# Performance work log

Hardware: AMD Instinct MI355X
Metric: run time of the kernel (lower is better)

Reference implementation:

```python
import jax, jax.numpy as jnp
import numpy as np

B, S, D, H = 4, 2048, 1024, 16
E = D // H  # head_size = 64


def setup_inputs() -> dict:
    key = jax.random.key(0)
    ks = jax.random.split(key, 6)
    scale = 1.0 / np.sqrt(D)
    embedded = jax.random.normal(ks[0], (B, S, D), dtype=jnp.float32)
    # Per-head Q/K/V projection weights, stacked over heads: [H, D, E]
    Wq = jax.random.normal(ks[1], (H, D, E), dtype=jnp.float32) * scale
    Wk = jax.random.normal(ks[2], (H, D, E), dtype=jnp.float32) * scale
    Wv = jax.random.normal(ks[3], (H, D, E), dtype=jnp.float32) * scale
    # Output projection (nn.Linear(model_dim, model_dim))
    Wo = jax.random.normal(ks[4], (D, D), dtype=jnp.float32) * scale
    bo = jax.random.normal(ks[5], (D,), dtype=jnp.float32) * scale
    return {"embedded": embedded, "Wq": Wq, "Wk": Wk, "Wv": Wv, "Wo": Wo, "bo": bo}


def reference(embedded, Wq, Wk, Wv, Wo, bo):
    # Batched over heads instead of the original Python loop; same math.
    q = jnp.einsum('bsd,hde->bhse', embedded, Wq)  # [B,H,S,E]
    k = jnp.einsum('bsd,hde->bhse', embedded, Wk)
    v = jnp.einsum('bsd,hde->bhse', embedded, Wv)
    scores = jnp.einsum('bhse,bhte->bhst', q, k) / jnp.sqrt(jnp.float32(E))
    causal = jnp.tril(jnp.ones((S, S), dtype=bool))  # [S,S]
    scores = jnp.where(causal, scores, jnp.float32(-jnp.inf))
    attn = jax.nn.softmax(scores, axis=-1)  # [B,H,S,S]
    out = jnp.einsum('bhst,bhte->bhse', attn, v)  # [B,H,S,E]
    # concat heads along last dim: [B,S,H*E] == [B,S,D]
    out = out.transpose(0, 2, 1, 3).reshape(B, S, D)
    # output projection (dropout is identity in eval mode)
    return out @ Wo.T + bo
```

## Files before the change

### kernel.cpp

```cpp
#include <hip/hip_runtime.h>
#include <hip/hip_bf16.h>

#define B_ 4
#define S_ 2048
#define D_ 1024
#define H_ 16
#define E_ 64
#define M_ (B_*S_)
#define NQKV_ 3072

typedef __attribute__((ext_vector_type(8))) short bf16x8;
typedef __attribute__((ext_vector_type(4))) float f32x4;
typedef __attribute__((ext_vector_type(16))) float f32x16;
typedef __attribute__((ext_vector_type(4))) unsigned short u16x4;
typedef unsigned short u16;

#define QSCALE 0.18033688011f
#define AS1 __attribute__((address_space(1)))
#define AS3 __attribute__((address_space(3)))

#define SWZ(r) ((((r) & 7) ^ ((((r) >> 3) & 3) << 1)) << 4)

static __device__ __forceinline__ u16 f2bf(float f) {
  unsigned u = __builtin_bit_cast(unsigned, f);
  unsigned r = (u + 0x7FFFu + ((u >> 16) & 1u)) >> 16;
  return (u16)r;
}

static __device__ __forceinline__ unsigned pk2(float a, float b) {
  unsigned r;
  asm("v_cvt_pk_bf16_f32 %0, %1, %2" : "=v"(r) : "v"(a), "v"(b));
  return r;
}


__global__ __launch_bounds__(256) void cvt_fused(const float* __restrict__ emb,
                                                 const float* __restrict__ Wo,
                                                 const float* __restrict__ Wq,
                                                 const float* __restrict__ Wk,
                                                 const float* __restrict__ Wv,
                                                 u16* __restrict__ X,
                                                 u16* __restrict__ WoT,
                                                 u16* __restrict__ Wt) {
  __shared__ float t[64][65];
  const int bid = blockIdx.x;
  const int tid = threadIdx.x;
  if (bid < 8192) {
    int i = bid * 256 + tid;
    f32x4 v = ((const f32x4*)emb)[i];
    u16x4 o;
    o.x = f2bf(v.x); o.y = f2bf(v.y); o.z = f2bf(v.z); o.w = f2bf(v.w);
    ((u16x4*)X)[i] = o;
  } else if (bid < 9216) {
    int i = (bid - 8192) * 256 + tid;
    f32x4 v = ((const f32x4*)Wo)[i];
    u16x4 o;
    o.x = f2bf(v.x); o.y = f2bf(v.y); o.z = f2bf(v.z); o.w = f2bf(v.w);
    ((u16x4*)WoT)[i] = o;
  } else {
    const int blk = bid - 9216;
    const int h = blk >> 4;
    const int db = (blk & 15) * 64;
    const float* srcs[3] = {Wq, Wk, Wv};
#pragma unroll
    for (int m = 0; m < 3; ++m) {
      const float* src = srcs[m] + (size_t)h * 65536 + (size_t)db * 64;
      __syncthreads();
#pragma unroll
      for (int i = 0; i < 16; ++i) {
        int idx = i * 256 + tid;
        int d = idx >> 6, e = idx & 63;
        t[e][d] = src[d * 64 + e];
      }
      __syncthreads();
      u16* dst = Wt + (size_t)(m * 1024 + h * 64) * 1024 + db;
#pragma unroll
      for (int i = 0; i < 16; ++i) {
        int idx = i * 256 + tid;
        int e = idx >> 6, d = idx & 63;
        dst[(size_t)e * 1024 + d] = f2bf(t[e][d]);
      }
    }
  }
}


__global__ __launch_bounds__(512, 2) void gemm_qkv(const u16* __restrict__ A,
                                                   const u16* __restrict__ Bt,
                                                   u16* __restrict__ QK,
                                                   u16* __restrict__ Vt) {
  __shared__ u16 As[3][256 * 32];
  __shared__ u16 Bs[3][384 * 32];
  const int tid = threadIdx.x;
  const int lane = tid & 63, wv = tid >> 6;
  const int ll = lane & 15, lg = lane >> 4;
  const int wm = wv >> 2, wn = wv & 3;
  const int bm = blockIdx.x, bn = blockIdx.y;

  const int sr = tid >> 2;
  const int scb = (tid & 3) * 16;
  const char* a0 = (const char*)(A + (size_t)(bm * 256 + sr) * 1024) + scb;
  const char* a1 = (const char*)(A + (size_t)(bm * 256 + 128 + sr) * 1024) + scb;
  const char* b0 = (const char*)(Bt + (size_t)(bn * 384 + sr) * 1024) + scb;
  const char* b1 = (const char*)(Bt + (size_t)(bn * 384 + 128 + sr) * 1024) + scb;
  const char* b2 = (const char*)(Bt + (size_t)(bn * 384 + 256 + sr) * 1024) + scb;

  auto stage = [&](int t, int bi) {
    const size_t adv = (size_t)t * 64;
    char* ad = (char*)&As[bi][0] + tid * 16;
    char* bd = (char*)&Bs[bi][0] + tid * 16;
    __builtin_amdgcn_global_load_lds((const AS1 void*)(a0 + adv), (AS3 void*)ad, 16, 0, 0);
    __builtin_amdgcn_global_load_lds((const AS1 void*)(a1 + adv), (AS3 void*)(ad + 8192), 16, 0, 0);
    __builtin_amdgcn_global_load_lds((const AS1 void*)(b0 + adv), (AS3 void*)bd, 16, 0, 0);
    __builtin_amdgcn_global_load_lds((const AS1 void*)(b1 + adv), (AS3 void*)(bd + 8192), 16, 0, 0);
    __builtin_amdgcn_global_load_lds((const AS1 void*)(b2 + adv), (AS3 void*)(bd + 16384), 16, 0, 0);
  };

  f32x4 acc[8][6] = {};

  stage(0, 0);
  stage(1, 1);
  for (int t = 0; t < 32; ++t) {
    const int cur = t % 3;
    if (t + 2 < 32) {
      stage(t + 2, (t + 2) % 3);
      asm volatile("s_waitcnt vmcnt(10)" ::: "memory");
    } else if (t + 1 < 32) {
      asm volatile("s_waitcnt vmcnt(5)" ::: "memory");
    } else {
      asm volatile("s_waitcnt vmcnt(0)" ::: "memory");
    }
    __builtin_amdgcn_s_barrier();

    const char* ab = (const char*)&As[cur][0];
    const char* bb = (const char*)&Bs[cur][0];

    bf16x8 bf[6];
#pragma unroll
    for (int ni = 0; ni < 6; ++ni) {
      int row = wn * 96 + ni * 16 + ll;
      bf[ni] = *(const bf16x8*)(bb + row * 64 + lg * 16);
    }
    __builtin_amdgcn_s_setprio(1);
#pragma unroll
    for (int mi = 0; mi < 8; ++mi) {
      int row = wm * 128 + mi * 16 + ll;
      bf16x8 af = *(const bf16x8*)(ab + row * 64 + lg * 16);
#pragma unroll
      for (int ni = 0; ni < 6; ++ni)
        acc[mi][ni] = __builtin_amdgcn_mfma_f32_16x16x32_bf16(
            af, bf[ni], acc[mi][ni], 0, 0, 0);
    }
    __builtin_amdgcn_s_setprio(0);
    __builtin_amdgcn_s_barrier();
  }

  const int sig = (((lg & 1) << 1) | (lg >> 1)) << 2;
#pragma unroll
  for (int mi = 0; mi < 8; ++mi) {
#pragma unroll
    for (int ni = 0; ni < 6; ++ni) {
      int c = bn * 384 + wn * 96 + ni * 16 + ll;
      int r0 = bm * 256 + wm * 128 + mi * 16 + lg * 4;
      if (c >= 2048) {
        int bb2 = r0 >> 11, s0 = r0 & 2047;
        int s0p = (s0 & ~15) | sig;
        u16x4 pkv;
        pkv.x = f2bf(acc[mi][ni][0]); pkv.y = f2bf(acc[mi][ni][1]);
        pkv.z = f2bf(acc[mi][ni][2]); pkv.w = f2bf(acc[mi][ni][3]);
        *(u16x4*)&Vt[((size_t)(bb2 * 1024 + (c - 2048))) * 2048 + s0p] = pkv;
      } else {
        const float qs = (c < 1024) ? QSCALE : 1.0f;
#pragma unroll
        for (int j = 0; j < 4; ++j)
          QK[(size_t)(r0 + j) * 2048 + c] = f2bf(acc[mi][ni][j] * qs);
      }
    }
  }
}


__global__ __launch_bounds__(512, 2) void gemm_out(const u16* __restrict__ A,
                                                   const u16* __restrict__ Bt,
                                                   float* __restrict__ C,
                                                   const float* __restrict__ bias) {
  __shared__ u16 As[3][256 * 32];
  __shared__ u16 Bs[3][128 * 32];
  const int tid = threadIdx.x;
  const int lane = tid & 63, wv = tid >> 6;
  const int ll = lane & 15, lg = lane >> 4;
  const int wm = wv >> 2, wn = wv & 3;
  const int bm = blockIdx.x, bn = blockIdx.y;

  const int sr = tid >> 2;
  const int scb = (tid & 3) * 16;
  const char* a0 = (const char*)(A + (size_t)(bm * 256 + sr) * 1024) + scb;
  const char* a1 = (const char*)(A + (size_t)(bm * 256 + 128 + sr) * 1024) + scb;
  const char* b0 = (const char*)(Bt + (size_t)(bn * 128 + sr) * 1024) + scb;

  auto stage = [&](int t, int bi) {
    const size_t adv = (size_t)t * 64;
    char* ad = (char*)&As[bi][0] + tid * 16;
    char* bd = (char*)&Bs[bi][0] + tid * 16;
    __builtin_amdgcn_global_load_lds((const AS1 void*)(a0 + adv), (AS3 void*)ad, 16, 0, 0);
    __builtin_amdgcn_global_load_lds((const AS1 void*)(a1 + adv), (AS3 void*)(ad + 8192), 16, 0, 0);
    __builtin_amdgcn_global_load_lds((const AS1 void*)(b0 + adv), (AS3 void*)bd, 16, 0, 0);
  };

  f32x4 acc[8][2] = {};

  stage(0, 0);
  stage(1, 1);
  for (int t = 0; t < 32; ++t) {
    const int cur = t % 3;
    if (t + 2 < 32) {
      stage(t + 2, (t + 2) % 3);
      asm volatile("s_waitcnt vmcnt(6)" ::: "memory");
    } else if (t + 1 < 32) {
      asm volatile("s_waitcnt vmcnt(3)" ::: "memory");
    } else {
      asm volatile("s_waitcnt vmcnt(0)" ::: "memory");
    }
    __builtin_amdgcn_s_barrier();

    const char* ab = (const char*)&As[cur][0];
    const char* bb = (const char*)&Bs[cur][0];

    bf16x8 bf[2];
#pragma unroll
    for (int ni = 0; ni < 2; ++ni) {
      int row = wn * 32 + ni * 16 + ll;
      bf[ni] = *(const bf16x8*)(bb + row * 64 + lg * 16);
    }
    __builtin_amdgcn_s_setprio(1);
#pragma unroll
    for (int mi = 0; mi < 8; ++mi) {
      int row = wm * 128 + mi * 16 + ll;
      bf16x8 af = *(const bf16x8*)(ab + row * 64 + lg * 16);
#pragma unroll
      for (int ni = 0; ni < 2; ++ni)
        acc[mi][ni] = __builtin_amdgcn_mfma_f32_16x16x32_bf16(
            af, bf[ni], acc[mi][ni], 0, 0, 0);
    }
    __builtin_amdgcn_s_setprio(0);
    __builtin_amdgcn_s_barrier();
  }

#pragma unroll
  for (int mi = 0; mi < 8; ++mi) {
#pragma unroll
    for (int ni = 0; ni < 2; ++ni) {
      int c = bn * 128 + wn * 32 + ni * 16 + ll;
      int r0 = bm * 256 + wm * 128 + mi * 16 + lg * 4;
      float bv = bias[c];
#pragma unroll
      for (int j = 0; j < 4; ++j)
        C[(size_t)(r0 + j) * 1024 + c] = acc[mi][ni][j] + bv;
    }
  }
}


__global__ __launch_bounds__(512, 2) void attn(const u16* __restrict__ QK,
                                               const u16* __restrict__ Vt,
                                               u16* __restrict__ AO) {
  __shared__ u16 Klds[4][4096];
  __shared__ u16 Vlds[4][4096];

  const int wg = blockIdx.x;
  const int lin = (wg & 7) * 32 + (wg >> 3);
  const int bh = lin >> 2, pr = lin & 3;
  const int b = bh >> 4, h = bh & 15;
  const int tid = threadIdx.x;
  const int lane = tid & 63, wv = tid >> 6;
  const int lq = lane & 31, hi = lane >> 5;

  const int srow = tid >> 3;
  const int scolb = ((tid & 7) * 16) ^ SWZ(srow);
  const char* ksrc = (const char*)(QK + (size_t)(b * S_ + srow) * 2048 + 1024 + h * E_) + scolb;
  const char* vsrc = (const char*)(Vt + (size_t)(bh * 64 + srow) * 2048) + scolb;

  const int nktA = 4 * pr + 4;
  const int NS = 36;

  auto stage = [&](int sq, int kb) {
    char* kd = (char*)&Klds[0][0] + (sq & 3) * 8192 + wv * 1024;
    char* vd = (char*)&Vlds[0][0] + (sq & 3) * 8192 + wv * 1024;
    __builtin_amdgcn_global_load_lds((const AS1 void*)(ksrc + (size_t)kb * 4096),
                                     (AS3 void*)kd, 16, 0, 0);
    __builtin_amdgcn_global_load_lds((const AS1 void*)(vsrc + kb * 2),
                                     (AS3 void*)vd, 16, 0, 0);
  };

  stage(0, 0);
  stage(1, (1 < nktA ? 1 : 1 - nktA) * 64);

  int seq = 0;
  for (int ph = 0; ph < 2; ++ph) {
    const int qt = ph ? 7 - pr : pr;
    const int nkt = 4 * qt + 4;
    const int qw0 = qt * 256 + wv * 32;
    const int q = qw0 + lq;

    const u16* qp = QK + (size_t)(b * S_ + q) * 2048 + h * E_;
    bf16x8 qf[4];
#pragma unroll
    for (int c = 0; c < 4; ++c)
      qf[c] = *(const bf16x8*)(qp + c * 16 + hi * 8);

    float m_run = -INFINITY, l_part = 0.f;
    f32x16 o0 = {}, o1 = {};

    for (int kt = 0; kt < nkt; ++kt, ++seq) {
      if (seq + 2 < NS) {
        int s2 = seq + 2;
        stage(s2, (s2 < nktA ? s2 : s2 - nktA) * 64);
      }
      if (seq < NS - 2)       asm volatile("s_waitcnt vmcnt(4)" ::: "memory");
      else if (seq == NS - 2) asm volatile("s_waitcnt vmcnt(2)" ::: "memory");
      else                    asm volatile("s_waitcnt vmcnt(0)" ::: "memory");
      __builtin_amdgcn_s_barrier();

      const int kb = kt * 64;
      if (kb > qw0 + 31) continue;
      const char* kbuf = (const char*)&Klds[0][0] + (seq & 3) * 8192;
      const char* vbuf = (const char*)&Vlds[0][0] + (seq & 3) * 8192;

      auto half = [&](int kb2) __attribute__((always_inline)) {
        f32x16 sc = {};
        __builtin_amdgcn_s_setprio(1);
        const int krow = kb2 * 32 + lq;
#pragma unroll
        for (int c = 0; c < 4; ++c) {
          bf16x8 kf = *(const bf16x8*)(kbuf + krow * 128 +
                                       ((c * 32 + hi * 16) ^ SWZ(krow)));
          sc = __builtin_amdgcn_mfma_f32_32x32x16_bf16(kf, qf[c], sc, 0, 0, 0);
        }
        __builtin_amdgcn_s_setprio(0);

        if (kb + kb2 * 32 + 31 > qw0) {
#pragma unroll
          for (int r = 0; r < 16; ++r) {
            int key = kb + kb2 * 32 + (r & 3) + 8 * (r >> 2) + 4 * hi;
            if (key > q) sc[r] = -1e30f;
          }
        }

        float pm = sc[0];
#pragma unroll
        for (int r = 1; r < 16; ++r) pm = fmaxf(pm, sc[r]);
        if (__any(pm - m_run > 8.0f)) {
          float g = fmaxf(pm, __shfl_xor(pm, 32, 64));
          float mn = fmaxf(m_run, g);
          float corr = exp2f(m_run - mn);
          m_run = mn;
          l_part *= corr;
          o0 *= corr;
          o1 *= corr;
        }

        float p[16];
#pragma unroll
        for (int r = 0; r < 16; ++r) {
          p[r] = exp2f(sc[r] - m_run);
          l_part += p[r];
        }
        __builtin_amdgcn_s_setprio(1);
#pragma unroll
        for (int gg = 0; gg < 2; ++gg) {
          union { unsigned w[4]; bf16x8 v; } pf;
          pf.w[0] = pk2(p[gg * 8 + 0], p[gg * 8 + 1]);
          pf.w[1] = pk2(p[gg * 8 + 2], p[gg * 8 + 3]);
          pf.w[2] = pk2(p[gg * 8 + 4], p[gg * 8 + 5]);
          pf.w[3] = pk2(p[gg * 8 + 6], p[gg * 8 + 7]);
          const int g = kb2 * 2 + gg;
          {
            bf16x8 vf = *(const bf16x8*)(vbuf + lq * 128 +
                                         ((g * 32 + hi * 16) ^ SWZ(lq)));
            o0 = __builtin_amdgcn_mfma_f32_32x32x16_bf16(vf, pf.v, o0, 0, 0, 0);
          }
          {
            const int er = 32 + lq;
            bf16x8 vf = *(const bf16x8*)(vbuf + er * 128 +
                                         ((g * 32 + hi * 16) ^ SWZ(er)));
            o1 = __builtin_amdgcn_mfma_f32_32x32x16_bf16(vf, pf.v, o1, 0, 0, 0);
          }
        }
        __builtin_amdgcn_s_setprio(0);
      };

      half(0);
      if (kb + 32 <= qw0 + 31) half(1);
    }

    float l = l_part + __shfl_xor(l_part, 32, 64);
    float rl = 1.0f / l;

#pragma unroll
    for (int qd = 0; qd < 4; ++qd) {
      u16x4 w0, w1;
#pragma unroll
      for (int j = 0; j < 4; ++j) {
        w0[j] = f2bf(o0[qd * 4 + j] * rl);
        w1[j] = f2bf(o1[qd * 4 + j] * rl);
      }
      const size_t base = (size_t)(b * S_ + q) * D_ + h * E_ + 8 * qd + 4 * hi;
      *(u16x4*)&AO[base] = w0;
      *(u16x4*)&AO[base + 32] = w1;
    }
  }
}


extern "C" void kernel_launch(void* const* d_in, const int* in_sizes, int n_in,
                              void* d_out, int out_size, void* d_ws, size_t ws_size,
                              hipStream_t stream) {
  const float* embedded = (const float*)d_in[0];
  const float* Wq = (const float*)d_in[1];
  const float* Wk = (const float*)d_in[2];
  const float* Wv = (const float*)d_in[3];
  const float* Wo = (const float*)d_in[4];
  const float* bo = (const float*)d_in[5];
  float* out = (float*)d_out;

  char* ws = (char*)d_ws;
  u16* X    = (u16*)(ws);
  u16* Wqkv = (u16*)(ws + (16u << 20));
  u16* WoT  = (u16*)(ws + (22u << 20));
  u16* QK   = (u16*)(ws + (24u << 20));
  u16* Vt   = (u16*)(ws + (56u << 20));
  u16* AO   = (u16*)(ws + (72u << 20));

  cvt_fused<<<9472, 256, 0, stream>>>(embedded, Wo, Wq, Wk, Wv, X, WoT, Wqkv);
  gemm_qkv<<<dim3(32, 8), 512, 0, stream>>>(X, Wqkv, QK, Vt);
  attn<<<256, 512, 0, stream>>>(QK, Vt, AO);
  gemm_out<<<dim3(32, 8), 512, 0, stream>>>(AO, WoT, out, bo);
}
```

Baseline: 181.0 us.

## Retile QKV and output GEMMs with 32x32 MFMA and swizzled LDS

Both GEMMs switch from 16x16x32 to 32x32x16 MFMA instructions. LDS reads now use an XOR swizzle applied at global-load time to avoid bank conflicts. The QKV GEMM tile shrinks from 256x384 to 256x128, giving 768 blocks with higher occupancy. The output GEMM moves to 128x128 tiles with 256 threads, giving 512 blocks. Fewer registers per wave and more blocks aim to fill the CUs better and cut LDS stalls, at the cost of less operand reuse per block and more global traffic.

```diff
diff --git a/kernel.cpp b/kernel.cpp
--- a/kernel.cpp
+++ b/kernel.cpp
@@ -20,6 +20,7 @@
 #define AS3 __attribute__((address_space(3)))
 
 #define SWZ(r) ((((r) & 7) ^ ((((r) >> 3) & 3) << 1)) << 4)
+#define SWZ64(r) (((((r) & 3) ^ (((r) >> 2) & 3))) << 4)
 
 static __device__ __forceinline__ u16 f2bf(float f) {
   unsigned u = __builtin_bit_cast(unsigned, f);
@@ -85,118 +86,23 @@
 }
 
 
-__global__ __launch_bounds__(512, 2) void gemm_qkv(const u16* __restrict__ A,
+__global__ __launch_bounds__(512, 4) void gemm_qkv(const u16* __restrict__ A,
                                                    const u16* __restrict__ Bt,
                                                    u16* __restrict__ QK,
                                                    u16* __restrict__ Vt) {
   __shared__ u16 As[3][256 * 32];
-  __shared__ u16 Bs[3][384 * 32];
-  const int tid = threadIdx.x;
-  const int lane = tid & 63, wv = tid >> 6;
-  const int ll = lane & 15, lg = lane >> 4;
-  const int wm = wv >> 2, wn = wv & 3;
-  const int bm = blockIdx.x, bn = blockIdx.y;
-
-  const int sr = tid >> 2;
-  const int scb = (tid & 3) * 16;
-  const char* a0 = (const char*)(A + (size_t)(bm * 256 + sr) * 1024) + scb;
-  const char* a1 = (const char*)(A + (size_t)(bm * 256 + 128 + sr) * 1024) + scb;
-  const char* b0 = (const char*)(Bt + (size_t)(bn * 384 + sr) * 1024) + scb;
-  const char* b1 = (const char*)(Bt + (size_t)(bn * 384 + 128 + sr) * 1024) + scb;
-  const char* b2 = (const char*)(Bt + (size_t)(bn * 384 + 256 + sr) * 1024) + scb;
-
-  auto stage = [&](int t, int bi) {
-    const size_t adv = (size_t)t * 64;
-    char* ad = (char*)&As[bi][0] + tid * 16;
-    char* bd = (char*)&Bs[bi][0] + tid * 16;
-    __builtin_amdgcn_global_load_lds((const AS1 void*)(a0 + adv), (AS3 void*)ad, 16, 0, 0);
-    __builtin_amdgcn_global_load_lds((const AS1 void*)(a1 + adv), (AS3 void*)(ad + 8192), 16, 0, 0);
-    __builtin_amdgcn_global_load_lds((const AS1 void*)(b0 + adv), (AS3 void*)bd, 16, 0, 0);
-    __builtin_amdgcn_global_load_lds((const AS1 void*)(b1 + adv), (AS3 void*)(bd + 8192), 16, 0, 0);
-    __builtin_amdgcn_global_load_lds((const AS1 void*)(b2 + adv), (AS3 void*)(bd + 16384), 16, 0, 0);
-  };
-
-  f32x4 acc[8][6] = {};
-
-  stage(0, 0);
-  stage(1, 1);
-  for (int t = 0; t < 32; ++t) {
-    const int cur = t % 3;
-    if (t + 2 < 32) {
-      stage(t + 2, (t + 2) % 3);
-      asm volatile("s_waitcnt vmcnt(10)" ::: "memory");
-    } else if (t + 1 < 32) {
-      asm volatile("s_waitcnt vmcnt(5)" ::: "memory");
-    } else {
-      asm volatile("s_waitcnt vmcnt(0)" ::: "memory");
-    }
-    __builtin_amdgcn_s_barrier();
-
-    const char* ab = (const char*)&As[cur][0];
-    const char* bb = (const char*)&Bs[cur][0];
-
-    bf16x8 bf[6];
-#pragma unroll
-    for (int ni = 0; ni < 6; ++ni) {
-      int row = wn * 96 + ni * 16 + ll;
-      bf[ni] = *(const bf16x8*)(bb + row * 64 + lg * 16);
-    }
-    __builtin_amdgcn_s_setprio(1);
-#pragma unroll
-    for (int mi = 0; mi < 8; ++mi) {
-      int row = wm * 128 + mi * 16 + ll;
-      bf16x8 af = *(const bf16x8*)(ab + row * 64 + lg * 16);
-#pragma unroll
-      for (int ni = 0; ni < 6; ++ni)
-        acc[mi][ni] = __builtin_amdgcn_mfma_f32_16x16x32_bf16(
-            af, bf[ni], acc[mi][ni], 0, 0, 0);
-    }
-    __builtin_amdgcn_s_setprio(0);
-    __builtin_amdgcn_s_barrier();
-  }
-
-  const int sig = (((lg & 1) << 1) | (lg >> 1)) << 2;
-#pragma unroll
-  for (int mi = 0; mi < 8; ++mi) {
-#pragma unroll
-    for (int ni = 0; ni < 6; ++ni) {
-      int c = bn * 384 + wn * 96 + ni * 16 + ll;
-      int r0 = bm * 256 + wm * 128 + mi * 16 + lg * 4;
-      if (c >= 2048) {
-        int bb2 = r0 >> 11, s0 = r0 & 2047;
-        int s0p = (s0 & ~15) | sig;
-        u16x4 pkv;
-        pkv.x = f2bf(acc[mi][ni][0]); pkv.y = f2bf(acc[mi][ni][1]);
-        pkv.z = f2bf(acc[mi][ni][2]); pkv.w = f2bf(acc[mi][ni][3]);
-        *(u16x4*)&Vt[((size_t)(bb2 * 1024 + (c - 2048))) * 2048 + s0p] = pkv;
-      } else {
-        const float qs = (c < 1024) ? QSCALE : 1.0f;
-#pragma unroll
-        for (int j = 0; j < 4; ++j)
-          QK[(size_t)(r0 + j) * 2048 + c] = f2bf(acc[mi][ni][j] * qs);
-      }
-    }
-  }
-}
-
-
-__global__ __launch_bounds__(512, 2) void gemm_out(const u16* __restrict__ A,
-                                                   const u16* __restrict__ Bt,
-                                                   float* __restrict__ C,
-                                                   const float* __restrict__ bias) {
-  __shared__ u16 As[3][256 * 32];
   __shared__ u16 Bs[3][128 * 32];
   const int tid = threadIdx.x;
   const int lane = tid & 63, wv = tid >> 6;
-  const int ll = lane & 15, lg = lane >> 4;
-  const int wm = wv >> 2, wn = wv & 3;
+  const int lq = lane & 31, hi = lane >> 5;
+  const int wm = wv >> 1, wn = wv & 1;
   const int bm = blockIdx.x, bn = blockIdx.y;
 
-  const int sr = tid >> 2;
-  const int scb = (tid & 3) * 16;
-  const char* a0 = (const char*)(A + (size_t)(bm * 256 + sr) * 1024) + scb;
-  const char* a1 = (const char*)(A + (size_t)(bm * 256 + 128 + sr) * 1024) + scb;
-  const char* b0 = (const char*)(Bt + (size_t)(bn * 128 + sr) * 1024) + scb;
+  const int srow = tid >> 2;
+  const int scb = ((tid & 3) * 16) ^ SWZ64(srow);
+  const char* a0 = (const char*)(A + (size_t)(bm * 256 + srow) * 1024) + scb;
+  const char* a1 = (const char*)(A + (size_t)(bm * 256 + 128 + srow) * 1024) + scb;
+  const char* b0 = (const char*)(Bt + (size_t)(bn * 128 + srow) * 1024) + scb;
 
   auto stage = [&](int t, int bi) {
     const size_t adv = (size_t)t * 64;
@@ -207,7 +113,7 @@
     __builtin_amdgcn_global_load_lds((const AS1 void*)(b0 + adv), (AS3 void*)bd, 16, 0, 0);
   };
 
-  f32x4 acc[8][2] = {};
+  f32x16 acc[2][2] = {};
 
   stage(0, 0);
   stage(1, 1);
@@ -226,36 +132,160 @@
     const char* ab = (const char*)&As[cur][0];
     const char* bb = (const char*)&Bs[cur][0];
 
-    bf16x8 bf[2];
+    bf16x8 af[2][2], bfr[2][2];
+#pragma unroll
+    for (int mi = 0; mi < 2; ++mi) {
+      int row = wm * 64 + mi * 32 + lq;
+#pragma unroll
+      for (int ks = 0; ks < 2; ++ks)
+        af[mi][ks] = *(const bf16x8*)(ab + row * 64 +
+                                      ((ks * 32 + hi * 16) ^ SWZ64(row)));
+    }
 #pragma unroll
     for (int ni = 0; ni < 2; ++ni) {
-      int row = wn * 32 + ni * 16 + ll;
-      bf[ni] = *(const bf16x8*)(bb + row * 64 + lg * 16);
+      int row = wn * 64 + ni * 32 + lq;
+#pragma unroll
+      for (int ks = 0; ks < 2; ++ks)
+        bfr[ni][ks] = *(const bf16x8*)(bb + row * 64 +
+                                       ((ks * 32 + hi * 16) ^ SWZ64(row)));
     }
     __builtin_amdgcn_s_setprio(1);
 #pragma unroll
-    for (int mi = 0; mi < 8; ++mi) {
-      int row = wm * 128 + mi * 16 + ll;
-      bf16x8 af = *(const bf16x8*)(ab + row * 64 + lg * 16);
-#pragma unroll
-      for (int ni = 0; ni < 2; ++ni)
-        acc[mi][ni] = __builtin_amdgcn_mfma_f32_16x16x32_bf16(
-            af, bf[ni], acc[mi][ni], 0, 0, 0);
-    }
+    for (int ks = 0; ks < 2; ++ks)
+#pragma unroll
+      for (int mi = 0; mi < 2; ++mi)
+#pragma unroll
+        for (int ni = 0; ni < 2; ++ni)
+          acc[mi][ni] = __builtin_amdgcn_mfma_f32_32x32x16_bf16(
+              af[mi][ks], bfr[ni][ks], acc[mi][ni], 0, 0, 0);
     __builtin_amdgcn_s_setprio(0);
     __builtin_amdgcn_s_barrier();
   }
 
 #pragma unroll
-  for (int mi = 0; mi < 8; ++mi) {
+  for (int mi = 0; mi < 2; ++mi) {
 #pragma unroll
     for (int ni = 0; ni < 2; ++ni) {
-      int c = bn * 128 + wn * 32 + ni * 16 + ll;
-      int r0 = bm * 256 + wm * 128 + mi * 16 + lg * 4;
-      float bv = bias[c];
-#pragma unroll
-      for (int j = 0; j < 4; ++j)
-        C[(size_t)(r0 + j) * 1024 + c] = acc[mi][ni][j] + bv;
+      const int colg = bn * 128 + wn * 64 + ni * 32 + lq;
+      const int r0 = bm * 256 + wm * 64 + mi * 32;
+      if (colg >= 2048) {
+        const int e = colg - 2048;
+#pragma unroll
+        for (int q4 = 0; q4 < 4; ++q4) {
+          int tok = r0 + 8 * q4 + 4 * hi;
+          int bb2 = tok >> 11, s0 = tok & 2047;
+          int blk = (s0 >> 2) & 3;
+          int s0p = (s0 & ~15) | ((((blk & 1) << 1) | (blk >> 1)) << 2);
+          u16x4 pkv;
+          pkv.x = f2bf(acc[mi][ni][q4 * 4 + 0]);
+          pkv.y = f2bf(acc[mi][ni][q4 * 4 + 1]);
+          pkv.z = f2bf(acc[mi][ni][q4 * 4 + 2]);
+          pkv.w = f2bf(acc[mi][ni][q4 * 4 + 3]);
+          *(u16x4*)&Vt[((size_t)(bb2 * 1024 + e)) * 2048 + s0p] = pkv;
+        }
+      } else {
+        const float qs = (colg < 1024) ? QSCALE : 1.0f;
+#pragma unroll
+        for (int r = 0; r < 16; ++r) {
+          int row = r0 + (r & 3) + 8 * (r >> 2) + 4 * hi;
+          QK[(size_t)row * 2048 + colg] = f2bf(acc[mi][ni][r] * qs);
+        }
+      }
+    }
+  }
+}
+
+
+__global__ __launch_bounds__(256, 3) void gemm_out(const u16* __restrict__ A,
+                                                   const u16* __restrict__ Bt,
+                                                   float* __restrict__ C,
+                                                   const float* __restrict__ bias) {
+  __shared__ u16 As[3][128 * 32];
+  __shared__ u16 Bs[3][128 * 32];
+  const int tid = threadIdx.x;
+  const int lane = tid & 63, wv = tid >> 6;
+  const int lq = lane & 31, hi = lane >> 5;
+  const int wm = wv >> 1, wn = wv & 1;
+  const int bm = blockIdx.x, bn = blockIdx.y;
+
+  const int srow = tid >> 2;
+  const int scb0 = ((tid & 3) * 16) ^ SWZ64(srow);
+  const char* a0 = (const char*)(A + (size_t)(bm * 128 + srow) * 1024) + scb0;
+  const char* a1 = (const char*)(A + (size_t)(bm * 128 + 64 + srow) * 1024) + scb0;
+  const char* b0 = (const char*)(Bt + (size_t)(bn * 128 + srow) * 1024) + scb0;
+  const char* b1 = (const char*)(Bt + (size_t)(bn * 128 + 64 + srow) * 1024) + scb0;
+
+  auto stage = [&](int t, int bi) {
+    const size_t adv = (size_t)t * 64;
+    char* ad = (char*)&As[bi][0] + tid * 16;
+    char* bd = (char*)&Bs[bi][0] + tid * 16;
+    __builtin_amdgcn_global_load_lds((const AS1 void*)(a0 + adv), (AS3 void*)ad, 16, 0, 0);
+    __builtin_amdgcn_global_load_lds((const AS1 void*)(a1 + adv), (AS3 void*)(ad + 4096), 16, 0, 0);
+    __builtin_amdgcn_global_load_lds((const AS1 void*)(b0 + adv), (AS3 void*)bd, 16, 0, 0);
+    __builtin_amdgcn_global_load_lds((const AS1 void*)(b1 + adv), (AS3 void*)(bd + 4096), 16, 0, 0);
+  };
+
+  f32x16 acc[2][2] = {};
+
+  stage(0, 0);
+  stage(1, 1);
+  for (int t = 0; t < 32; ++t) {
+    const int cur = t % 3;
+    if (t + 2 < 32) {
+      stage(t + 2, (t + 2) % 3);
+      asm volatile("s_waitcnt vmcnt(8)" ::: "memory");
+    } else if (t + 1 < 32) {
+      asm volatile("s_waitcnt vmcnt(4)" ::: "memory");
+    } else {
+      asm volatile("s_waitcnt vmcnt(0)" ::: "memory");
+    }
+    __builtin_amdgcn_s_barrier();
+
+    const char* ab = (const char*)&As[cur][0];
+    const char* bb = (const char*)&Bs[cur][0];
+
+    bf16x8 af[2][2], bfr[2][2];
+#pragma unroll
+    for (int mi = 0; mi < 2; ++mi) {
+      int row = wm * 64 + mi * 32 + lq;
+#pragma unroll
+      for (int ks = 0; ks < 2; ++ks)
+        af[mi][ks] = *(const bf16x8*)(ab + row * 64 +
+                                      ((ks * 32 + hi * 16) ^ SWZ64(row)));
+    }
+#pragma unroll
+    for (int ni = 0; ni < 2; ++ni) {
+      int row = wn * 64 + ni * 32 + lq;
+#pragma unroll
+      for (int ks = 0; ks < 2; ++ks)
+        bfr[ni][ks] = *(const bf16x8*)(bb + row * 64 +
+                                       ((ks * 32 + hi * 16) ^ SWZ64(row)));
+    }
+    __builtin_amdgcn_s_setprio(1);
+#pragma unroll
+    for (int ks = 0; ks < 2; ++ks)
+#pragma unroll
+      for (int mi = 0; mi < 2; ++mi)
+#pragma unroll
+        for (int ni = 0; ni < 2; ++ni)
+          acc[mi][ni] = __builtin_amdgcn_mfma_f32_32x32x16_bf16(
+              af[mi][ks], bfr[ni][ks], acc[mi][ni], 0, 0, 0);
+    __builtin_amdgcn_s_setprio(0);
+    __builtin_amdgcn_s_barrier();
+  }
+
+#pragma unroll
+  for (int mi = 0; mi < 2; ++mi) {
+#pragma unroll
+    for (int ni = 0; ni < 2; ++ni) {
+      const int colg = bn * 128 + wn * 64 + ni * 32 + lq;
+      const int r0 = bm * 128 + wm * 64 + mi * 32;
+      const float bv = bias[colg];
+#pragma unroll
+      for (int r = 0; r < 16; ++r) {
+        int row = r0 + (r & 3) + 8 * (r >> 2) + 4 * hi;
+        C[(size_t)row * 1024 + colg] = acc[mi][ni][r] + bv;
+      }
     }
   }
 }
@@ -432,7 +462,7 @@
   u16* AO   = (u16*)(ws + (72u << 20));
 
   cvt_fused<<<9472, 256, 0, stream>>>(embedded, Wo, Wq, Wk, Wv, X, WoT, Wqkv);
-  gemm_qkv<<<dim3(32, 8), 512, 0, stream>>>(X, Wqkv, QK, Vt);
+  gemm_qkv<<<dim3(32, 24), 512, 0, stream>>>(X, Wqkv, QK, Vt);
   attn<<<256, 512, 0, stream>>>(QK, Vt, AO);
-  gemm_out<<<dim3(32, 8), 512, 0, stream>>>(AO, WoT, out, bo);
-}
+  gemm_out<<<dim3(64, 8), 256, 0, stream>>>(AO, WoT, out, bo);
+}
```

New measurement: 175.9 us. 2.8% less time.
